# Kernel optimization log

Hardware: AMD Instinct MI355X
Metric: run time of the kernel (lower is better)

Reference implementation:

```python
import jax, jax.numpy as jnp
import numpy as np

B, N, P_FEATS = 8, 4096, 3
WIDTH, HEADS, LAYERS, N_LAT = 768, 12, 8, 256
NUM_FREQS = 8
D_HEAD = WIDTH // HEADS
SCALE = 1.0 / np.sqrt(np.sqrt(D_HEAD))  # applied to q and k separately
IN_DIM = 3 * (1 + 2 * NUM_FREQS) + P_FEATS  # 54
EPS = 1e-5


def fourier_embed(pc):
    # pc: [B,N,3] -> [B,N,51] (include_input + sin/cos at freqs 2^0..2^7)
    freqs = (2.0 ** jnp.arange(NUM_FREQS)).astype(pc.dtype)
    ang = pc[..., None] * freqs  # [B,N,3,F]
    ang = ang.reshape(*pc.shape[:-1], 3 * NUM_FREQS)
    return jnp.concatenate([pc, jnp.sin(ang), jnp.cos(ang)], axis=-1)


def layernorm(x, s, b):
    mu = jnp.mean(x, axis=-1, keepdims=True)
    var = jnp.mean(jnp.square(x - mu), axis=-1, keepdims=True)
    return (x - mu) * jax.lax.rsqrt(var + EPS) * s + b


def mh_attn(q, k, v):
    # q: [B,T,H,C], k/v: [B,S,H,C]
    w = jnp.einsum('bthc,bshc->bhts', q * SCALE, k * SCALE)
    w = jax.nn.softmax(w.astype(jnp.float32), axis=-1).astype(q.dtype)
    out = jnp.einsum('bhts,bshc->bthc', w, v)
    return out.reshape(*q.shape[:2], -1)


def setup_inputs() -> dict:
    key = jax.random.key(0)
    ks = iter(jax.random.split(key, 64))
    rn = lambda shape, std=0.02: jax.random.normal(next(ks), shape, jnp.float32) * std
    inp = {
        'pc': jax.random.normal(next(ks), (B, N, 3), jnp.float32),
        'feats': jax.random.uniform(next(ks), (B, N, P_FEATS), jnp.float32),
        'query': rn((N_LAT, WIDTH)),
        'in_W': rn((WIDTH, IN_DIM)), 'in_b': jnp.zeros((WIDTH,)),
        'ca_qkv_W': rn((3 * WIDTH, WIDTH)), 'ca_qkv_b': jnp.zeros((3 * WIDTH,)),
        'ca_proj_W': rn((WIDTH, WIDTH)), 'ca_proj_b': jnp.zeros((WIDTH,)),
        'ln1_s': jnp.ones((LAYERS, WIDTH)), 'ln1_b': jnp.zeros((LAYERS, WIDTH)),
        'qkv_W': rn((LAYERS, 3 * WIDTH, WIDTH)), 'qkv_b': jnp.zeros((LAYERS, 3 * WIDTH)),
        'proj_W': rn((LAYERS, WIDTH, WIDTH)), 'proj_b': jnp.zeros((LAYERS, WIDTH)),
        'ln2_s': jnp.ones((LAYERS, WIDTH)), 'ln2_b': jnp.zeros((LAYERS, WIDTH)),
        'fc_W': rn((LAYERS, 4 * WIDTH, WIDTH)), 'fc_b': jnp.zeros((LAYERS, 4 * WIDTH)),
        'fc2_W': rn((LAYERS, WIDTH, 4 * WIDTH)), 'fc2_b': jnp.zeros((LAYERS, WIDTH)),
    }
    return inp


def _forward(pc, feats, query, in_W, in_b, ca_qkv_W, ca_qkv_b, ca_proj_W, ca_proj_b,
             ln1_s, ln1_b, qkv_W, qkv_b, proj_W, proj_b, ln2_s, ln2_b,
             fc_W, fc_b, fc2_W, fc2_b):
    bs = pc.shape[0]
    data = jnp.concatenate([fourier_embed(pc), feats], axis=-1)  # [B,N,54]
    data = data @ in_W.T + in_b  # [B,N,W]
    q_lat = jnp.broadcast_to(query[None], (bs, N_LAT, WIDTH))

    # --- cross attention (no residual, matching source) ---
    q = (q_lat @ ca_qkv_W.T + ca_qkv_b)[..., :WIDTH]
    kv = data @ ca_qkv_W.T + ca_qkv_b
    k, v = kv[..., WIDTH:2 * WIDTH], kv[..., 2 * WIDTH:]
    q = q.reshape(bs, N_LAT, HEADS, D_HEAD)
    k = k.reshape(bs, N, HEADS, D_HEAD)
    v = v.reshape(bs, N, HEADS, D_HEAD)
    latents = mh_attn(q, k, v) @ ca_proj_W.T + ca_proj_b  # [B,L,W]

    # --- self-attention transformer stack via scan ---
    def block(x, p):
        (l1s, l1b, qW, qb, pW, pb, l2s, l2b, fW, fb, f2W, f2b) = p
        h = layernorm(x, l1s, l1b)
        qkv = (h @ qW.T + qb).reshape(bs, N_LAT, HEADS, 3 * D_HEAD)
        qh, kh, vh = jnp.split(qkv, 3, axis=-1)
        x = x + mh_attn(qh, kh, vh) @ pW.T + pb
        h = layernorm(x, l2s, l2b)
        h = jax.nn.gelu(h @ fW.T + fb, approximate=False) @ f2W.T + f2b
        return x + h, None

    params = (ln1_s, ln1_b, qkv_W, qkv_b, proj_W, proj_b, ln2_s, ln2_b, fc_W, fc_b, fc2_W, fc2_b)
    latents, _ = jax.lax.scan(block, latents, params)
    return latents, pc


def reference(pc, feats, query, in_W, in_b, ca_qkv_W, ca_qkv_b, ca_proj_W, ca_proj_b,
              ln1_s, ln1_b, qkv_W, qkv_b, proj_W, proj_b, ln2_s, ln2_b,
              fc_W, fc_b, fc2_W, fc2_b):
    return _forward(pc, feats, query, in_W, in_b, ca_qkv_W, ca_qkv_b, ca_proj_W, ca_proj_b,
                    ln1_s, ln1_b, qkv_W, qkv_b, proj_W, proj_b, ln2_s, ln2_b,
                    fc_W, fc_b, fc2_W, fc2_b)
```

## Files before the change

kernel.cpp:

```cpp
#include <hip/hip_runtime.h>
#include <stdint.h>

typedef unsigned short u16;
typedef __bf16 bf16x8 __attribute__((ext_vector_type(8)));
typedef float f32x4 __attribute__((ext_vector_type(4)));

#define DEVINL __device__ __forceinline__

DEVINL u16 f2bf(float f) {
  union { float f; unsigned u; } c; c.f = f;
  unsigned u = c.u + 0x7FFFu + ((c.u >> 16) & 1u);
  return (u16)(u >> 16);
}

DEVINL float bf2f(u16 v) {
  union { unsigned u; float f; } c; c.u = (unsigned)v << 16;
  return c.f;
}

DEVINL unsigned pk2bf(float a, float b) {
#if __has_builtin(__builtin_amdgcn_cvt_pk_bf16_f32)
  auto r = __builtin_amdgcn_cvt_pk_bf16_f32(a, b);
  unsigned u;
  __builtin_memcpy(&u, &r, 4);
  return u;
#else
  return (unsigned)f2bf(a) | ((unsigned)f2bf(b) << 16);
#endif
}

DEVINL void gl2lds16(const void* g, void* l) {
  __builtin_amdgcn_global_load_lds(
      (const __attribute__((address_space(1))) unsigned int*)g,
      (__attribute__((address_space(3))) unsigned int*)l, 16, 0, 0);
}

__global__ __launch_bounds__(256) void cvt4_kernel(
    const float* __restrict__ s0, u16* __restrict__ d0, int n0,
    const float* __restrict__ s1, u16* __restrict__ d1, int n1,
    const float* __restrict__ s2, u16* __restrict__ d2, int n2,
    const float* __restrict__ s3, u16* __restrict__ d3, int n3) {
  int i = blockIdx.x * 256 + threadIdx.x;
  const float* s; u16* d;
  if (i < n0) { s = s0; d = d0; }
  else {
    i -= n0;
    if (i < n1) { s = s1; d = d1; }
    else {
      i -= n1;
      if (i < n2) { s = s2; d = d2; }
      else {
        i -= n2;
        if (i >= n3) return;
        s = s3; d = d3;
      }
    }
  }
  float4 v = ((const float4*)s)[i];
  ((uint2*)d)[i] = make_uint2(pk2bf(v.x, v.y), pk2bf(v.z, v.w));
}

__global__ __launch_bounds__(256) void pad_inwT_kernel(const float* __restrict__ src,
                                                       u16* __restrict__ dst) {
  int t = blockIdx.x * 256 + threadIdx.x;
  if (t >= 64 * 768) return;
  int j = t / 768, o = t - j * 768;
  dst[t] = (j < 54) ? f2bf(src[o * 54 + j]) : (u16)0;
}

__global__ __launch_bounds__(256) void bprime_kernel(const float* __restrict__ caW,
                                                     const float* __restrict__ caB,
                                                     const float* __restrict__ inb,
                                                     float* __restrict__ bp) {
  int w = threadIdx.x >> 6, lane = threadIdx.x & 63;
  int m = blockIdx.x * 4 + w;
  const float* row = caW + (size_t)(768 + m) * 768;
  float s = 0.f;
#pragma unroll
  for (int k = 0; k < 12; k++) s += row[lane + k * 64] * inb[lane + k * 64];
#pragma unroll
  for (int msk = 32; msk >= 1; msk >>= 1) s += __shfl_xor(s, msk, 64);
  if (lane == 0) bp[m] = s + caB[768 + m];
}

__global__ __launch_bounds__(256) void embed_kernel(const float* __restrict__ pc,
                                                    const float* __restrict__ feats,
                                                    u16* __restrict__ emb) {
  int t = blockIdx.x * 256 + threadIdx.x;
  int p = t >> 6, c = t & 63;
  float v = 0.f;
  if (c < 3) {
    v = pc[p * 3 + c];
  } else if (c < 27) {
    int i = c - 3;
    float f = (float)(1 << (i & 7));
    v = sinf(pc[p * 3 + (i >> 3)] * f);
  } else if (c < 51) {
    int i = c - 27;
    float f = (float)(1 << (i & 7));
    v = cosf(pc[p * 3 + (i >> 3)] * f);
  } else if (c < 54) {
    v = feats[p * 3 + (c - 51)];
  }
  emb[t] = f2bf(v);
}

template <int TM, int TN, int WR, int WC, int MODE>
__global__ __launch_bounds__(256) void gemm_t(
    const u16* __restrict__ A, const u16* __restrict__ Bw,
    const float* __restrict__ bias, const float* __restrict__ resid,
    float* __restrict__ outF, u16* __restrict__ outB,
    int M, int N, int Nout, int K, int gelu,
    u16* __restrict__ vt, int vy, int skvt, int bsh) {
  constexpr int IM = TM / WR / 16;
  constexpr int IN = TN / WC / 16;
  __shared__ u16 As[2][TM * 32];
  __shared__ u16 Bs[2][TN * 32];
  const int tid = threadIdx.x;
  const int lane = tid & 63, w = tid >> 6;
  const int l15 = lane & 15, quad = lane >> 4;
  const int mblk = blockIdx.x * TM, nblk = blockIdx.y * TN;
  const int wm = (w % WR) * (TM / WR);
  const int wn = (w / WR) * (TN / WC);

  f32x4 acc[IM][IN];
#pragma unroll
  for (int i = 0; i < IM; i++)
#pragma unroll
    for (int j = 0; j < IN; j++) acc[i][j] = f32x4{0.f, 0.f, 0.f, 0.f};

  bool tv = false;
  if (MODE == 1) tv = ((int)blockIdx.y >= vy);
  if (MODE == 2) tv = ((int)(blockIdx.y % 3) == 2);

  auto stage = [&](int bi, int k0) {
#pragma unroll
    for (int s = tid; s < TM * 4; s += 256) {
      int row = s >> 2, c8 = (s & 3) << 3;
      gl2lds16(A + (size_t)(mblk + row) * K + (k0 + c8), &As[bi][s * 8]);
    }
#pragma unroll
    for (int s = tid; s < TN * 4; s += 256) {
      int row = s >> 2, c8 = (s & 3) << 3;
      gl2lds16(Bw + (size_t)(nblk + row) * K + (k0 + c8), &Bs[bi][s * 8]);
    }
  };

  if (!tv) {
    stage(0, 0);
    __syncthreads();
    int cur = 0;
    for (int k0 = 0; k0 < K; k0 += 32) {
      if (k0 + 32 < K) stage(cur ^ 1, k0 + 32);
      bf16x8 af[IM], bfr[IN];
#pragma unroll
      for (int i = 0; i < IM; i++)
        af[i] = *(const bf16x8*)&As[cur][(wm + i * 16 + l15) * 32 + quad * 8];
#pragma unroll
      for (int j = 0; j < IN; j++)
        bfr[j] = *(const bf16x8*)&Bs[cur][(wn + j * 16 + l15) * 32 + quad * 8];
#pragma unroll
      for (int i = 0; i < IM; i++)
#pragma unroll
        for (int j = 0; j < IN; j++)
          acc[i][j] = __builtin_amdgcn_mfma_f32_16x16x32_bf16(bfr[j], af[i], acc[i][j], 0, 0, 0);
      __syncthreads();
      cur ^= 1;
    }
#pragma unroll
    for (int i = 0; i < IM; i++) {
      int m = mblk + wm + i * 16 + l15;
#pragma unroll
      for (int j = 0; j < IN; j++) {
        int n0 = nblk + wn + j * 16 + quad * 4;
        float4 bv = bias ? *(const float4*)&bias[n0] : make_float4(0.f, 0.f, 0.f, 0.f);
        float v0 = acc[i][j][0] + bv.x;
        float v1 = acc[i][j][1] + bv.y;
        float v2 = acc[i][j][2] + bv.z;
        float v3 = acc[i][j][3] + bv.w;
        if (gelu) {
          v0 = 0.5f * v0 * (1.0f + erff(v0 * 0.70710678118f));
          v1 = 0.5f * v1 * (1.0f + erff(v1 * 0.70710678118f));
          v2 = 0.5f * v2 * (1.0f + erff(v2 * 0.70710678118f));
          v3 = 0.5f * v3 * (1.0f + erff(v3 * 0.70710678118f));
        }
        size_t idx = (size_t)m * Nout + n0;
        if (resid) {
          float4 rv = *(const float4*)&resid[idx];
          v0 += rv.x; v1 += rv.y; v2 += rv.z; v3 += rv.w;
        }
        if (outF) {
          float4 ov = {v0, v1, v2, v3};
          *(float4*)&outF[idx] = ov;
        }
        if (outB) {
          *(uint2*)&outB[idx] = make_uint2(pk2bf(v0, v1), pk2bf(v2, v3));
        }
      }
    }
  } else {
    stage(0, 0);
    __syncthreads();
    int cur = 0;
    for (int k0 = 0; k0 < K; k0 += 32) {
      if (k0 + 32 < K) stage(cur ^ 1, k0 + 32);
      bf16x8 af[IM], bfr[IN];
#pragma unroll
      for (int i = 0; i < IM; i++)
        af[i] = *(const bf16x8*)&As[cur][(wm + i * 16 + l15) * 32 + quad * 8];
#pragma unroll
      for (int j = 0; j < IN; j++)
        bfr[j] = *(const bf16x8*)&Bs[cur][(wn + j * 16 + l15) * 32 + quad * 8];
#pragma unroll
      for (int i = 0; i < IM; i++)
#pragma unroll
        for (int j = 0; j < IN; j++)
          acc[i][j] = __builtin_amdgcn_mfma_f32_16x16x32_bf16(af[i], bfr[j], acc[i][j], 0, 0, 0);
      __syncthreads();
      cur ^= 1;
    }
    int msk = (1 << bsh) - 1;
#pragma unroll
    for (int j = 0; j < IN; j++) {
      int n = nblk + wn + j * 16 + l15;
      float bv = bias ? bias[n] : 0.f;
#pragma unroll
      for (int i = 0; i < IM; i++) {
        int m0 = mblk + wm + i * 16 + quad * 4;
        int b = m0 >> bsh;
        int s0 = m0 & msk;
        float v0 = acc[i][j][0] + bv;
        float v1 = acc[i][j][1] + bv;
        float v2 = acc[i][j][2] + bv;
        float v3 = acc[i][j][3] + bv;
        size_t vrow;
        if (MODE == 2) {
          int h = blockIdx.y / 3;
          vrow = (size_t)(b * 12 + h) * 64 + (wn + j * 16 + l15);
        } else {
          vrow = (size_t)b * 768 + (n - vy * TN);
        }
        size_t addr = vrow * skvt + s0;
        *(uint2*)&vt[addr] = make_uint2(pk2bf(v0, v1), pk2bf(v2, v3));
      }
    }
  }
}

__global__ __launch_bounds__(256) void flash_kernel(
    const u16* __restrict__ Q, long qb, int qrs, int qhs,
    const u16* __restrict__ Kp, long kb, int krs, int khs,
    const u16* __restrict__ Vt, u16* __restrict__ Out,
    u16* __restrict__ Part, float* __restrict__ Ml,
    int Skv, int nsplit, int kvlen, int nbh, float scale2) {
  __shared__ u16 Qs[64 * 64];
  __shared__ u16 Ks[2][64 * 64];
  __shared__ u16 Vs[2][64 * 64];
  __shared__ u16 Ps[64 * 72];

  const int tid = threadIdx.x;
  const int lane = tid & 63, w = tid >> 6;
  const int l15 = lane & 15, quad = lane >> 4;

  int bid = blockIdx.x;
  int grp = nbh * nsplit;
  int qt = bid / grp;
  int rem = bid - qt * grp;
  int bh = rem / nsplit;
  int split = rem - bh * nsplit;
  int h = bh % 12, b = bh / 12;

  const u16* Qbase = Q + (size_t)b * qb + (size_t)(qt * 64) * qrs + h * qhs;
  const u16* Kbase = Kp + (size_t)b * kb + (size_t)h * khs;
  const u16* Vbase = Vt + ((size_t)(b * 12 + h) * 64) * Skv;

  int kt0 = split * kvlen;

#pragma unroll
  for (int p = 0; p < 2; ++p) {
    int slot = tid + p * 256;
    int row = slot >> 3, c = slot & 7;
    int cg = (c - row) & 7;
    gl2lds16(Qbase + (size_t)row * qrs + cg * 8, &Qs[slot * 8]);
    gl2lds16(Kbase + (size_t)(kt0 + row) * krs + cg * 8, &Ks[0][slot * 8]);
    gl2lds16(Vbase + (size_t)row * Skv + kt0 + cg * 8, &Vs[0][slot * 8]);
  }
  __syncthreads();

  bf16x8 qa[2];
#pragma unroll
  for (int kk = 0; kk < 2; kk++)
    qa[kk] = *(const bf16x8*)&Qs[(w * 16 + l15) * 64 + ((kk * 4 + quad + l15) & 7) * 8];

  f32x4 zero = {0.f, 0.f, 0.f, 0.f};
  f32x4 O[4];
#pragma unroll
  for (int d = 0; d < 4; d++) O[d] = zero;
  float m_i = -1e30f, l_i = 0.f;

  int cur = 0;
  for (int kt = kt0; kt < kt0 + kvlen; kt += 64) {
    if (kt + 64 < kt0 + kvlen) {
#pragma unroll
      for (int p = 0; p < 2; ++p) {
        int slot = tid + p * 256;
        int row = slot >> 3, c = slot & 7;
        int cg = (c - row) & 7;
        gl2lds16(Kbase + (size_t)(kt + 64 + row) * krs + cg * 8, &Ks[cur ^ 1][slot * 8]);
        gl2lds16(Vbase + (size_t)row * Skv + (kt + 64) + cg * 8, &Vs[cur ^ 1][slot * 8]);
      }
    }

    f32x4 St[4];
#pragma unroll
    for (int j = 0; j < 4; j++) St[j] = zero;
#pragma unroll
    for (int kk = 0; kk < 2; kk++) {
#pragma unroll
      for (int j = 0; j < 4; j++) {
        bf16x8 kf = *(const bf16x8*)&Ks[cur][(j * 16 + l15) * 64 + ((kk * 4 + quad + l15) & 7) * 8];
        St[j] = __builtin_amdgcn_mfma_f32_16x16x32_bf16(kf, qa[kk], St[j], 0, 0, 0);
      }
    }

    float mx = St[0][0];
#pragma unroll
    for (int j = 0; j < 4; j++)
#pragma unroll
      for (int r = 0; r < 4; r++) mx = fmaxf(mx, St[j][r]);
    mx = fmaxf(mx, __shfl_xor(mx, 16, 64));
    mx = fmaxf(mx, __shfl_xor(mx, 32, 64));
    mx *= scale2;
    float mnew = fmaxf(m_i, mx);
    float al = __expf(m_i - mnew);
    m_i = mnew;
    float sum = 0.f;
#pragma unroll
    for (int j = 0; j < 4; j++) {
      float p0 = __expf(fmaf(St[j][0], scale2, -mnew));
      float p1 = __expf(fmaf(St[j][1], scale2, -mnew));
      float p2 = __expf(fmaf(St[j][2], scale2, -mnew));
      float p3 = __expf(fmaf(St[j][3], scale2, -mnew));
      sum += (p0 + p1) + (p2 + p3);
      *(uint2*)&Ps[(w * 16 + l15) * 72 + j * 16 + quad * 4] =
          make_uint2(pk2bf(p0, p1), pk2bf(p2, p3));
    }
    sum += __shfl_xor(sum, 16, 64);
    sum += __shfl_xor(sum, 32, 64);
    l_i = l_i * al + sum;

    float a0 = __shfl(al, quad * 20 + 0, 64);
    float a1 = __shfl(al, quad * 20 + 1, 64);
    float a2 = __shfl(al, quad * 20 + 2, 64);
    float a3 = __shfl(al, quad * 20 + 3, 64);
#pragma unroll
    for (int d = 0; d < 4; d++) {
      O[d][0] *= a0; O[d][1] *= a1; O[d][2] *= a2; O[d][3] *= a3;
    }
    __asm__ __volatile__("s_waitcnt lgkmcnt(0)" ::: "memory");
#pragma unroll
    for (int kk = 0; kk < 2; kk++) {
      bf16x8 pa = *(const bf16x8*)&Ps[(w * 16 + l15) * 72 + kk * 32 + quad * 8];
#pragma unroll
      for (int d = 0; d < 4; d++) {
        bf16x8 vf = *(const bf16x8*)&Vs[cur][(d * 16 + l15) * 64 + ((kk * 4 + quad + l15) & 7) * 8];
        O[d] = __builtin_amdgcn_mfma_f32_16x16x32_bf16(pa, vf, O[d], 0, 0, 0);
      }
    }
    __syncthreads();
    cur ^= 1;
  }

  float l0 = __shfl(l_i, quad * 20 + 0, 64);
  float l1 = __shfl(l_i, quad * 20 + 1, 64);
  float l2 = __shfl(l_i, quad * 20 + 2, 64);
  float l3 = __shfl(l_i, quad * 20 + 3, 64);

  if (nsplit == 1) {
    float inv0 = 1.f / l0, inv1 = 1.f / l1, inv2 = 1.f / l2, inv3 = 1.f / l3;
    u16* Ob = Out + ((size_t)(b * 256 + qt * 64 + w * 16 + quad * 4)) * 768 + h * 64 + l15;
#pragma unroll
    for (int d = 0; d < 4; d++) {
      Ob[(size_t)0 * 768 + d * 16] = f2bf(O[d][0] * inv0);
      Ob[(size_t)1 * 768 + d * 16] = f2bf(O[d][1] * inv1);
      Ob[(size_t)2 * 768 + d * 16] = f2bf(O[d][2] * inv2);
      Ob[(size_t)3 * 768 + d * 16] = f2bf(O[d][3] * inv3);
    }
  } else {
    float m0 = __shfl(m_i, quad * 20 + 0, 64);
    float m1 = __shfl(m_i, quad * 20 + 1, 64);
    float m2 = __shfl(m_i, quad * 20 + 2, 64);
    float m3 = __shfl(m_i, quad * 20 + 3, 64);
    u16* Pb = Part + ((size_t)(bh * 4 + qt) * nsplit + split) * 4096;
    int rowb = w * 16 + quad * 4;
#pragma unroll
    for (int d = 0; d < 4; d++) {
      Pb[(rowb + 0) * 64 + d * 16 + l15] = f2bf(O[d][0]);
      Pb[(rowb + 1) * 64 + d * 16 + l15] = f2bf(O[d][1]);
      Pb[(rowb + 2) * 64 + d * 16 + l15] = f2bf(O[d][2]);
      Pb[(rowb + 3) * 64 + d * 16 + l15] = f2bf(O[d][3]);
    }
    if (l15 == 0) {
      float* MlB = Ml + ((size_t)(bh * 4 + qt) * nsplit + split) * 128;
      MlB[rowb + 0] = m0; MlB[rowb + 1] = m1; MlB[rowb + 2] = m2; MlB[rowb + 3] = m3;
      MlB[64 + rowb + 0] = l0; MlB[64 + rowb + 1] = l1;
      MlB[64 + rowb + 2] = l2; MlB[64 + rowb + 3] = l3;
    }
  }
}

__global__ __launch_bounds__(256) void freduce_kernel(
    const u16* __restrict__ Part, const float* __restrict__ Ml,
    u16* __restrict__ Out, int nsplit) {
  int bid = blockIdx.x;
  int qt = bid & 3, bh = bid >> 2;
  int h = bh % 12, b = bh / 12;
  int tid = threadIdx.x;
  int r = tid >> 2, dc = tid & 3;
  const float* mlb = Ml + (size_t)(bh * 4 + qt) * nsplit * 128;
  float M = -1e30f;
  for (int s = 0; s < nsplit; s++) M = fmaxf(M, mlb[s * 128 + r]);
  float L = 0.f;
  float accv[16];
#pragma unroll
  for (int i = 0; i < 16; i++) accv[i] = 0.f;
  const u16* pb = Part + (size_t)(bh * 4 + qt) * nsplit * 4096 + r * 64 + dc * 16;
  for (int s = 0; s < nsplit; s++) {
    float wgt = __expf(mlb[s * 128 + r] - M);
    L += wgt * mlb[s * 128 + 64 + r];
    u16 tmp[16];
    *(uint4*)tmp = *(const uint4*)(pb + s * 4096);
    *(uint4*)(tmp + 8) = *(const uint4*)(pb + s * 4096 + 8);
#pragma unroll
    for (int i = 0; i < 16; i++) accv[i] += wgt * bf2f(tmp[i]);
  }
  float inv = 1.f / L;
  unsigned ot[8];
#pragma unroll
  for (int i = 0; i < 8; i++)
    ot[i] = pk2bf(accv[2 * i] * inv, accv[2 * i + 1] * inv);
  u16* ob = Out + ((size_t)(b * 256 + qt * 64 + r)) * 768 + h * 64 + dc * 16;
  *(uint4*)ob = *(uint4*)ot;
  *(uint4*)(ob + 8) = *(uint4*)(ot + 4);
}

__global__ __launch_bounds__(256) void ln_kernel(const float* __restrict__ X,
                                                 const float* __restrict__ sc,
                                                 const float* __restrict__ bi,
                                                 u16* __restrict__ Hout) {
  int row = blockIdx.x;
  int tid = threadIdx.x;
  const float* x = X + (size_t)row * 768;
  float v0 = x[tid], v1 = x[tid + 256], v2 = x[tid + 512];
  float s = v0 + v1 + v2;
  float q = v0 * v0 + v1 * v1 + v2 * v2;
#pragma unroll
  for (int m = 1; m < 64; m <<= 1) {
    s += __shfl_xor(s, m, 64);
    q += __shfl_xor(q, m, 64);
  }
  __shared__ float rs[4], rq[4];
  if ((tid & 63) == 0) { rs[tid >> 6] = s; rq[tid >> 6] = q; }
  __syncthreads();
  s = rs[0] + rs[1] + rs[2] + rs[3];
  q = rq[0] + rq[1] + rq[2] + rq[3];
  float mu = s * (1.f / 768.f);
  float var = q * (1.f / 768.f) - mu * mu;
  float rstd = rsqrtf(var + 1e-5f);
  u16* ho = Hout + (size_t)row * 768;
  ho[tid]       = f2bf((v0 - mu) * rstd * sc[tid]       + bi[tid]);
  ho[tid + 256] = f2bf((v1 - mu) * rstd * sc[tid + 256] + bi[tid + 256]);
  ho[tid + 512] = f2bf((v2 - mu) * rstd * sc[tid + 512] + bi[tid + 512]);
}

__global__ __launch_bounds__(256) void copy4_kernel(const float* __restrict__ src,
                                                    float* __restrict__ dst, int n4) {
  int i = blockIdx.x * 256 + threadIdx.x;
  if (i < n4) ((float4*)dst)[i] = ((const float4*)src)[i];
}

extern "C" void kernel_launch(void* const* d_in, const int* in_sizes, int n_in,
                              void* d_out, int out_size, void* d_ws, size_t ws_size,
                              hipStream_t stream) {
  const float* pc        = (const float*)d_in[0];
  const float* feats     = (const float*)d_in[1];
  const float* query     = (const float*)d_in[2];
  const float* in_W      = (const float*)d_in[3];
  const float* in_b      = (const float*)d_in[4];
  const float* ca_qkv_W  = (const float*)d_in[5];
  const float* ca_qkv_b  = (const float*)d_in[6];
  const float* ca_proj_W = (const float*)d_in[7];
  const float* ca_proj_b = (const float*)d_in[8];
  const float* ln1_s     = (const float*)d_in[9];
  const float* ln1_b     = (const float*)d_in[10];
  const float* qkv_W     = (const float*)d_in[11];
  const float* qkv_b     = (const float*)d_in[12];
  const float* proj_W    = (const float*)d_in[13];
  const float* proj_b    = (const float*)d_in[14];
  const float* ln2_s     = (const float*)d_in[15];
  const float* ln2_b     = (const float*)d_in[16];
  const float* fc_W      = (const float*)d_in[17];
  const float* fc_b      = (const float*)d_in[18];
  const float* fc2_W     = (const float*)d_in[19];
  const float* fc2_b     = (const float*)d_in[20];

  char* base = (char*)d_ws;
  size_t off = 0;
  auto alloc = [&](size_t bytes) -> char* {
    char* p = base + off;
    off += (bytes + 255) & ~(size_t)255;
    return p;
  };

  u16* WqT     = (u16*)alloc(64 * 768 * 2);
  u16* Wquery  = (u16*)alloc(256 * 768 * 2);
  u16* Wcaqkv  = (u16*)alloc(2304 * 768 * 2);
  u16* Wcaproj = (u16*)alloc(768 * 768 * 2);
  u16* Wkp     = (u16*)alloc(1536 * 64 * 2);
  float* bprime = (float*)alloc(1536 * 4);
  u16* qc      = (u16*)alloc(256 * 768 * 2);
  u16* attn    = (u16*)alloc((size_t)2048 * 768 * 2);
  u16* hbuf    = (u16*)alloc((size_t)2048 * 768 * 2);
  char* uni    = alloc(13369344);
  u16* qkvb    = (u16*)uni;
  u16* VtS     = (u16*)(uni + 9437184);
  u16* fc1     = (u16*)uni;
  u16* Part    = (u16*)uni;
  float* Ml    = (float*)(uni + 12582912);

  size_t fixed_end = off;
  const size_t wAllSz = (size_t)8 * (2304 * 768 + 768 * 768 + 2 * 3072 * 768) * 2;
  auto crossSz = [](int cb) {
    return (size_t)cb * 4096 * 64 * 2 + 2 * ((size_t)cb * 4096 * 768 * 2);
  };

  bool allw; int CB;
  if (fixed_end + (wAllSz > crossSz(8) ? wAllSz : crossSz(8)) + 65536 <= ws_size) {
    allw = true;  CB = 8;
  } else if (fixed_end + 14155776 + crossSz(2) + 65536 <= ws_size) {
    allw = false; CB = 2;
  } else {
    allw = false; CB = 1;
  }

  u16 *WqkvB, *WprojB, *WfcB, *Wfc2B, *emb, *kvbK, *VtC;
  if (allw) {
    char* X = base + off;
    WqkvB  = (u16*)X;
    WprojB = WqkvB + (size_t)8 * 2304 * 768;
    WfcB   = WprojB + (size_t)8 * 768 * 768;
    Wfc2B  = WfcB + (size_t)8 * 3072 * 768;
    emb  = (u16*)X;
    kvbK = (u16*)(X + (size_t)CB * 4096 * 64 * 2);
    VtC  = (u16*)(X + (size_t)CB * 4096 * 64 * 2 + (size_t)CB * 4096 * 768 * 2);
  } else {
    WqkvB  = (u16*)alloc(2304 * 768 * 2);
    WprojB = (u16*)alloc(768 * 768 * 2);
    WfcB   = (u16*)alloc(3072 * 768 * 2);
    Wfc2B  = (u16*)alloc((size_t)768 * 3072 * 2);
    emb  = (u16*)alloc((size_t)CB * 4096 * 64 * 2);
    kvbK = (u16*)alloc((size_t)CB * 4096 * 768 * 2);
    VtC  = (u16*)alloc((size_t)CB * 4096 * 768 * 2);
  }

  float* latents = (float*)d_out;
  const float scale2 = 0.125f;

  {
    int n0 = 256 * 768 / 4, n1 = 2304 * 768 / 4, n2 = 768 * 768 / 4;
    cvt4_kernel<<<(n0 + n1 + n2 + 255) / 256, 256, 0, stream>>>(
        query, Wquery, n0, ca_qkv_W, Wcaqkv, n1, ca_proj_W, Wcaproj, n2,
        nullptr, nullptr, 0);
  }
  pad_inwT_kernel<<<192, 256, 0, stream>>>(in_W, WqT);
  gemm_t<64, 64, 2, 2, 0><<<dim3(24, 1), 256, 0, stream>>>(
      Wcaqkv + (size_t)768 * 768, WqT, nullptr, nullptr, nullptr, Wkp,
      1536, 64, 64, 768, 0, nullptr, 0, 0, 0);
  bprime_kernel<<<384, 256, 0, stream>>>(ca_qkv_W, ca_qkv_b, in_b, bprime);

  gemm_t<64, 64, 2, 2, 0><<<dim3(4, 12), 256, 0, stream>>>(
      Wquery, Wcaqkv, ca_qkv_b, nullptr, nullptr, qc,
      256, 768, 768, 768, 0, nullptr, 0, 0, 0);

  int nchunk = 8 / CB;
  for (int c = 0; c < nchunk; ++c) {
    int Mc = CB * 4096;
    const float* pc_c = pc + (size_t)c * Mc * 3;
    const float* ft_c = feats + (size_t)c * Mc * 3;
    embed_kernel<<<Mc / 4, 256, 0, stream>>>(pc_c, ft_c, emb);
    gemm_t<128, 128, 2, 2, 1><<<dim3(Mc / 128, 12), 256, 0, stream>>>(
        emb, Wkp, bprime, nullptr, nullptr, kvbK,
        Mc, 1536, 768, 64, 0, VtC, 6, 4096, 12);
    flash_kernel<<<CB * 12 * 16, 256, 0, stream>>>(
        qc, 0L, 768, 64, kvbK, (long)4096 * 768, 768, 64, VtC,
        nullptr, Part, Ml, 4096, 4, 1024, CB * 12, scale2);
    freduce_kernel<<<CB * 48, 256, 0, stream>>>(
        Part, Ml, attn + (size_t)c * CB * 256 * 768, 4);
  }
  gemm_t<64, 64, 2, 2, 0><<<dim3(32, 12), 256, 0, stream>>>(
      attn, Wcaproj, ca_proj_b, nullptr, latents, nullptr,
      2048, 768, 768, 768, 0, nullptr, 0, 0, 0);

  if (allw) {
    int n0 = 8 * 2304 * 768 / 4, n1 = 8 * 768 * 768 / 4, n2 = 8 * 3072 * 768 / 4;
    cvt4_kernel<<<(n0 + n1 + 2 * n2 + 255) / 256, 256, 0, stream>>>(
        qkv_W, WqkvB, n0, proj_W, WprojB, n1, fc_W, WfcB, n2, fc2_W, Wfc2B, n2);
  }

  for (int l = 0; l < 8; ++l) {
    u16* Wlq  = allw ? WqkvB  + (size_t)l * 2304 * 768 : WqkvB;
    u16* Wlp  = allw ? WprojB + (size_t)l * 768 * 768  : WprojB;
    u16* Wlf  = allw ? WfcB   + (size_t)l * 3072 * 768 : WfcB;
    u16* Wlf2 = allw ? Wfc2B  + (size_t)l * 3072 * 768 : Wfc2B;
    if (!allw) {
      int n0 = 2304 * 768 / 4, n1 = 768 * 768 / 4, n2 = 3072 * 768 / 4;
      cvt4_kernel<<<(n0 + n1 + 2 * n2 + 255) / 256, 256, 0, stream>>>(
          qkv_W + (size_t)l * 2304 * 768, Wlq, n0,
          proj_W + (size_t)l * 768 * 768, Wlp, n1,
          fc_W + (size_t)l * 3072 * 768, Wlf, n2,
          fc2_W + (size_t)l * 768 * 3072, Wlf2, n2);
    }
    ln_kernel<<<2048, 256, 0, stream>>>(latents, ln1_s + l * 768, ln1_b + l * 768, hbuf);
    gemm_t<64, 64, 2, 2, 2><<<dim3(32, 36), 256, 0, stream>>>(
        hbuf, Wlq, qkv_b + l * 2304, nullptr, nullptr, qkvb,
        2048, 2304, 2304, 768, 0, VtS, 0, 256, 8);
    flash_kernel<<<384, 256, 0, stream>>>(
        qkvb, (long)256 * 2304, 2304, 192, qkvb + 64, (long)256 * 2304, 2304, 192,
        VtS, attn, nullptr, nullptr, 256, 1, 256, 96, scale2);
    gemm_t<64, 64, 2, 2, 0><<<dim3(32, 12), 256, 0, stream>>>(
        attn, Wlp, proj_b + l * 768, latents, latents, nullptr,
        2048, 768, 768, 768, 0, nullptr, 0, 0, 0);
    ln_kernel<<<2048, 256, 0, stream>>>(latents, ln2_s + l * 768, ln2_b + l * 768, hbuf);
    gemm_t<64, 128, 1, 4, 0><<<dim3(32, 24), 256, 0, stream>>>(
        hbuf, Wlf, fc_b + l * 3072, nullptr, nullptr, fc1,
        2048, 3072, 3072, 768, 1, nullptr, 0, 0, 0);
    gemm_t<64, 64, 2, 2, 0><<<dim3(32, 12), 256, 0, stream>>>(
        fc1, Wlf2, fc2_b + l * 768, latents, latents, nullptr,
        2048, 768, 768, 3072, 0, nullptr, 0, 0, 0);
  }

  copy4_kernel<<<96, 256, 0, stream>>>(pc, (float*)d_out + (size_t)2048 * 768, 98304 / 4);
}
```

Baseline: 1.333 ms.

## Triple-buffer GEMM LDS staging with vmcnt waits and lighter attention barriers

The GEMM main loop moves from double to triple buffering of A/B tiles in LDS, with two stages prefetched ahead. Each iteration waits with a targeted s_waitcnt vmcnt instead of a full __syncthreads drain, so global-to-LDS loads for later tiles stay in flight during MFMA work. The two duplicated GEMM loops are merged into one with the MFMA operand order chosen inside. In the attention kernel, __syncthreads is replaced by explicit vmcnt waits plus a raw s_barrier so the next K/V tile's prefetch is not forced to complete early. The cost is 1.5x the LDS for GEMM tiles, which may reduce occupancy, and correctness now depends on the hand-counted vmcnt values.

```diff
diff --git a/kernel.cpp b/kernel.cpp
--- a/kernel.cpp
+++ b/kernel.cpp
@@ -33,6 +33,15 @@
   __builtin_amdgcn_global_load_lds(
       (const __attribute__((address_space(1))) unsigned int*)g,
       (__attribute__((address_space(3))) unsigned int*)l, 16, 0, 0);
+}
+
+template <int N> DEVINL void waitvm() {
+  asm volatile("s_waitcnt vmcnt(%0)" ::"n"(N) : "memory");
+}
+DEVINL void bar() {
+  asm volatile("" ::: "memory");
+  __builtin_amdgcn_s_barrier();
+  asm volatile("" ::: "memory");
 }
 
 __global__ __launch_bounds__(256) void cvt4_kernel(
@@ -114,8 +123,11 @@
     u16* __restrict__ vt, int vy, int skvt, int bsh) {
   constexpr int IM = TM / WR / 16;
   constexpr int IN = TN / WC / 16;
-  __shared__ u16 As[2][TM * 32];
-  __shared__ u16 Bs[2][TN * 32];
+  constexpr int PA = (TM * 4) / 256;
+  constexpr int PB = (TN * 4) / 256;
+  constexpr int PT = PA + PB;
+  __shared__ u16 As[3][TM * 32];
+  __shared__ u16 Bs[3][TN * 32];
   const int tid = threadIdx.x;
   const int lane = tid & 63, w = tid >> 6;
   const int l15 = lane & 15, quad = lane >> 4;
@@ -146,27 +158,41 @@
     }
   };
 
+  const int NT = K >> 5;
+  stage(0, 0);
+  if (NT > 1) stage(1, 32);
+
+  int cb = 0, sb = 2;
+  for (int i = 0; i < NT; ++i) {
+    if (i < NT - 1) waitvm<PT>(); else waitvm<0>();
+    bar();
+    if (i + 2 < NT) stage(sb, (i + 2) * 32);
+
+    bf16x8 af[IM], bfr[IN];
+#pragma unroll
+    for (int ii = 0; ii < IM; ii++)
+      af[ii] = *(const bf16x8*)&As[cb][(wm + ii * 16 + l15) * 32 + quad * 8];
+#pragma unroll
+    for (int jj = 0; jj < IN; jj++)
+      bfr[jj] = *(const bf16x8*)&Bs[cb][(wn + jj * 16 + l15) * 32 + quad * 8];
+    if (!tv) {
+#pragma unroll
+      for (int ii = 0; ii < IM; ii++)
+#pragma unroll
+        for (int jj = 0; jj < IN; jj++)
+          acc[ii][jj] = __builtin_amdgcn_mfma_f32_16x16x32_bf16(bfr[jj], af[ii], acc[ii][jj], 0, 0, 0);
+    } else {
+#pragma unroll
+      for (int ii = 0; ii < IM; ii++)
+#pragma unroll
+        for (int jj = 0; jj < IN; jj++)
+          acc[ii][jj] = __builtin_amdgcn_mfma_f32_16x16x32_bf16(af[ii], bfr[jj], acc[ii][jj], 0, 0, 0);
+    }
+    cb = (cb == 2) ? 0 : cb + 1;
+    sb = (sb == 2) ? 0 : sb + 1;
+  }
+
   if (!tv) {
-    stage(0, 0);
-    __syncthreads();
-    int cur = 0;
-    for (int k0 = 0; k0 < K; k0 += 32) {
-      if (k0 + 32 < K) stage(cur ^ 1, k0 + 32);
-      bf16x8 af[IM], bfr[IN];
-#pragma unroll
-      for (int i = 0; i < IM; i++)
-        af[i] = *(const bf16x8*)&As[cur][(wm + i * 16 + l15) * 32 + quad * 8];
-#pragma unroll
-      for (int j = 0; j < IN; j++)
-        bfr[j] = *(const bf16x8*)&Bs[cur][(wn + j * 16 + l15) * 32 + quad * 8];
-#pragma unroll
-      for (int i = 0; i < IM; i++)
-#pragma unroll
-        for (int j = 0; j < IN; j++)
-          acc[i][j] = __builtin_amdgcn_mfma_f32_16x16x32_bf16(bfr[j], af[i], acc[i][j], 0, 0, 0);
-      __syncthreads();
-      cur ^= 1;
-    }
 #pragma unroll
     for (int i = 0; i < IM; i++) {
       int m = mblk + wm + i * 16 + l15;
@@ -199,26 +225,6 @@
       }
     }
   } else {
-    stage(0, 0);
-    __syncthreads();
-    int cur = 0;
-    for (int k0 = 0; k0 < K; k0 += 32) {
-      if (k0 + 32 < K) stage(cur ^ 1, k0 + 32);
-      bf16x8 af[IM], bfr[IN];
-#pragma unroll
-      for (int i = 0; i < IM; i++)
-        af[i] = *(const bf16x8*)&As[cur][(wm + i * 16 + l15) * 32 + quad * 8];
-#pragma unroll
-      for (int j = 0; j < IN; j++)
-        bfr[j] = *(const bf16x8*)&Bs[cur][(wn + j * 16 + l15) * 32 + quad * 8];
-#pragma unroll
-      for (int i = 0; i < IM; i++)
-#pragma unroll
-        for (int j = 0; j < IN; j++)
-          acc[i][j] = __builtin_amdgcn_mfma_f32_16x16x32_bf16(af[i], bfr[j], acc[i][j], 0, 0, 0);
-      __syncthreads();
-      cur ^= 1;
-    }
     int msk = (1 << bsh) - 1;
 #pragma unroll
     for (int j = 0; j < IN; j++) {
@@ -300,7 +306,8 @@
 
   int cur = 0;
   for (int kt = kt0; kt < kt0 + kvlen; kt += 64) {
-    if (kt + 64 < kt0 + kvlen) {
+    bool hasnext = (kt + 64 < kt0 + kvlen);
+    if (hasnext) {
 #pragma unroll
       for (int p = 0; p < 2; ++p) {
         int slot = tid + p * 256;
@@ -309,7 +316,11 @@
         gl2lds16(Kbase + (size_t)(kt + 64 + row) * krs + cg * 8, &Ks[cur ^ 1][slot * 8]);
         gl2lds16(Vbase + (size_t)row * Skv + (kt + 64) + cg * 8, &Vs[cur ^ 1][slot * 8]);
       }
-    }
+      waitvm<4>();
+    } else {
+      waitvm<0>();
+    }
+    bar();
 
     f32x4 St[4];
 #pragma unroll
@@ -367,7 +378,7 @@
         O[d] = __builtin_amdgcn_mfma_f32_16x16x32_bf16(pa, vf, O[d], 0, 0, 0);
       }
     }
-    __syncthreads();
+    bar();
     cur ^= 1;
   }
 
```

Measured after the change: 1.367 ms. 2.5% more time.
